# Performance work log

Hardware: AMD Instinct MI355X
Metric: run time of the kernel (lower is better)

Reference implementation:

```python
import jax, jax.numpy as jnp
import numpy as np

D_MODEL = 512
D_INNER = 1024   # expand * d_model
NH = 16          # heads (headdim 64)
HD = 64
NS = 16          # d_state
HID = 1024       # ff hidden = expand * d_model


def _ln(x, w, b, eps=1e-5):
    m = x.mean(-1, keepdims=True)
    v = ((x - m) ** 2).mean(-1, keepdims=True)
    return (x - m) * jax.lax.rsqrt(v + eps) * w + b


def _rms(x, w, eps=1e-5):
    return x * jax.lax.rsqrt((x * x).mean(-1, keepdims=True) + eps) * w


def _tree_scan(dt, xh, Bv, Cv, pidx, A):
    # dt:[B,T,W,H] xh:[B,T,W,H,P] Bv,Cv:[B,T,W,N] pidx:[B,T,W] A:[H]
    B_, T, W, H = dt.shape
    P = xh.shape[-1]
    N = Bv.shape[-1]
    h0 = jnp.zeros((B_, W, H, P, N), dt.dtype)
    xs = (jnp.moveaxis(dt, 1, 0), jnp.moveaxis(xh, 1, 0),
          jnp.moveaxis(Bv, 1, 0), jnp.moveaxis(Cv, 1, 0),
          jnp.moveaxis(pidx, 1, 0))

    def step(h, inp):
        dt_t, xh_t, b_t, c_t, p_t = inp
        # gather parent state from previous level along the width axis
        hp = jnp.take_along_axis(h, p_t[:, :, None, None, None], axis=1)  # [B,W,H,P,N]
        dA = jnp.exp(dt_t * A)                                            # [B,W,H]
        h_new = dA[..., None, None] * hp \
              + dt_t[..., None, None] * xh_t[..., None] * b_t[:, :, None, None, :]
        y_t = jnp.einsum('bwhpn,bwn->bwhp', h_new, c_t)
        return h_new, y_t

    _, ys = jax.lax.scan(step, h0, xs)
    return jnp.moveaxis(ys, 0, 1)  # [B,T,W,H,P]


def setup_inputs() -> dict:
    key = jax.random.key(0)
    ks = jax.random.split(key, 12)
    B, T, W = 8, 64, 16
    d_in_proj = 2 * D_INNER + 2 * NS + NH  # z | x | B | C | dt
    inp = {
        'x': jax.random.normal(ks[0], (B, T, W, D_MODEL), jnp.float32),
        'parent_pos': jax.random.randint(ks[1], (B, T, W), 0, W, dtype=jnp.int32),
        'ln1_w': jnp.ones((D_MODEL,), jnp.float32),
        'ln1_b': jnp.zeros((D_MODEL,), jnp.float32),
        'in_w': jax.random.normal(ks[2], (D_MODEL, d_in_proj), jnp.float32) * 0.02,
        'in_b': jnp.zeros((d_in_proj,), jnp.float32),
        'A_log': jnp.log(jax.random.uniform(ks[3], (NH,), jnp.float32, 1.0, 16.0)),
        'dt_bias': jnp.full((NH,), -4.0, jnp.float32),
        'Dp': jnp.ones((NH,), jnp.float32),
        'norm_w': jnp.ones((D_INNER,), jnp.float32),
        'out_w': jax.random.normal(ks[4], (D_INNER, D_MODEL), jnp.float32) * 0.02,
        'out_b': jnp.zeros((D_MODEL,), jnp.float32),
        'ln2_w': jnp.ones((D_MODEL,), jnp.float32),
        'ln2_b': jnp.zeros((D_MODEL,), jnp.float32),
        'ff1_w': jax.random.normal(ks[5], (D_MODEL, 2 * HID), jnp.float32) * 0.02,
        'ff1_b': jnp.zeros((2 * HID,), jnp.float32),
        'ff2_w': jax.random.normal(ks[6], (HID, D_MODEL), jnp.float32) * 0.02,
        'ff2_b': jnp.zeros((D_MODEL,), jnp.float32),
    }
    return inp


def reference(x, parent_pos, ln1_w, ln1_b, in_w, in_b, A_log, dt_bias, Dp,
              norm_w, out_w, out_b, ln2_w, ln2_b, ff1_w, ff1_b, ff2_w, ff2_b):
    # norm1 + TreeMamba2 + residual
    xn = _ln(x, ln1_w, ln1_b)
    proj = xn @ in_w + in_b
    z, xp, Bv, Cv, dtr = jnp.split(
        proj, [D_INNER, 2 * D_INNER, 2 * D_INNER + NS, 2 * D_INNER + 2 * NS], axis=-1)
    dt = jax.nn.softplus(dtr + dt_bias)            # [B,T,W,NH]
    A = -jnp.exp(A_log)                            # [NH]
    xh = xp.reshape(*xp.shape[:-1], NH, HD)        # [B,T,W,NH,HD]
    y = _tree_scan(dt, xh, Bv, Cv, parent_pos, A)  # [B,T,W,NH,HD]
    y = y + Dp[..., None] * xh                     # skip connection D*x
    y = y.reshape(*y.shape[:-2], D_INNER)
    y = _rms(y * jax.nn.silu(z), norm_w)           # gated RMSNorm
    y = y @ out_w + out_b
    x = y + x
    # norm2 + gated FF + residual
    yn = _ln(x, ln2_w, ln2_b)
    f = yn @ ff1_w + ff1_b
    f1, g = jnp.split(f, 2, axis=-1)
    f = (f1 * jax.nn.silu(g)) @ ff2_w + ff2_b
    return x + f
```

## Files before the change

kernel.cpp:

```cpp
#include <hip/hip_runtime.h>
#include <hip/hip_bf16.h>
#include <cmath>

#define D_MODEL 512
#define D_INNER 1024
#define NHEAD 16
#define HDIM 64
#define NSTATE 16
#define NB 8
#define NT 64
#define NW 16
#define MROWS 8192
#define NPROJ 2096

typedef __attribute__((ext_vector_type(8))) short short8;
typedef __attribute__((ext_vector_type(4))) float f32x4;
typedef __hip_bfloat16 bf16;
typedef unsigned int u32;
typedef unsigned short u16;

__device__ __forceinline__ u32 fbits(float f) { return __float_as_uint(f); }
__device__ __forceinline__ float ubits(u32 u) { return __uint_as_float(u); }
__device__ __forceinline__ u32 pack_bf(float a, float b) {
  return (fbits(b) & 0xffff0000u) | (fbits(a) >> 16);
}

template<int N> __device__ __forceinline__ void vmwait() {
  if constexpr (N == 0)      asm volatile("s_waitcnt vmcnt(0)" ::: "memory");
  else if constexpr (N == 2) asm volatile("s_waitcnt vmcnt(2)" ::: "memory");
  else if constexpr (N == 3) asm volatile("s_waitcnt vmcnt(3)" ::: "memory");
  else if constexpr (N == 4) asm volatile("s_waitcnt vmcnt(4)" ::: "memory");
  else if constexpr (N == 6) asm volatile("s_waitcnt vmcnt(6)" ::: "memory");
  else if constexpr (N == 8) asm volatile("s_waitcnt vmcnt(8)" ::: "memory");
  else static_assert(N == 0, "unsupported vmcnt");
}

__device__ __forceinline__ void xcd_tile(int& bx, int& by) {
  int gx = gridDim.x;
  int nwg = gx * gridDim.y;
  int id = blockIdx.y * gx + blockIdx.x;
  int tile = (id & 7) * (nwg >> 3) + (id >> 3);
  bx = tile % gx;
  by = tile / gx;
}

__device__ __forceinline__ float block_sum(float v, float* sbuf) {
#pragma unroll
  for (int o = 32; o > 0; o >>= 1) v += __shfl_down(v, o, 64);
  int lane = threadIdx.x & 63, wid = threadIdx.x >> 6;
  if (lane == 0) sbuf[wid] = v;
  __syncthreads();
  if (threadIdx.x == 0) {
    float t = 0.f;
    for (int i = 0; i < 4; i++) t += sbuf[i];
    sbuf[0] = t;
  }
  __syncthreads();
  return sbuf[0];
}

__global__ __launch_bounds__(256) void ln512_bf16_kernel(
    const float* __restrict__ x, const float* __restrict__ w,
    const float* __restrict__ b, bf16* __restrict__ out) {
  __shared__ float s1[8], s2[8];
  int row = blockIdx.x;
  const float* xr = x + (size_t)row * D_MODEL;
  bf16* outr = out + (size_t)row * D_MODEL;
  int c0 = threadIdx.x, c1 = threadIdx.x + 256;
  float v0 = xr[c0], v1 = xr[c1];
  float s  = block_sum(v0 + v1, s1);
  float ss = block_sum(v0 * v0 + v1 * v1, s2);
  float mean = s * (1.f / 512.f);
  float var  = ss * (1.f / 512.f) - mean * mean;
  float inv  = rsqrtf(var + 1e-5f);
  outr[c0] = __float2bfloat16((v0 - mean) * inv * w[c0] + b[c0]);
  outr[c1] = __float2bfloat16((v1 - mean) * inv * w[c1] + b[c1]);
}

__global__ __launch_bounds__(256) void wconv_all_kernel(
    const float* __restrict__ in_w, bf16* __restrict__ in_wt,
    const float* __restrict__ out_w, bf16* __restrict__ out_wt,
    const float* __restrict__ ff1_w, bf16* __restrict__ ff1_wt,
    const float* __restrict__ ff2_w, bf16* __restrict__ ff2_wt) {
  __shared__ float tile[32][33];
  int id = blockIdx.x;
  const float* w; bf16* wt;
  int K, N, Npad, bx, by;
  if (id < 1088)      { w = in_w;  wt = in_wt;  K = 512;  N = NPROJ; Npad = 2176; bx = id % 68;  by = id / 68; }
  else if (id < 1600) { int j = id - 1088; w = out_w; wt = out_wt; K = 1024; N = 512;  Npad = 512;  bx = j % 16; by = j / 16; }
  else if (id < 2624) { int j = id - 1600; w = ff1_w; wt = ff1_wt; K = 512;  N = 2048; Npad = 2048; bx = j % 64; by = j / 64; }
  else                { int j = id - 2624; w = ff2_w; wt = ff2_wt; K = 1024; N = 512;  Npad = 512;  bx = j % 16; by = j / 16; }
  int n0 = bx * 32, k0 = by * 32;
  int tx = threadIdx.x & 31, ty = threadIdx.x >> 5;
#pragma unroll
  for (int i = 0; i < 4; i++) {
    int k = k0 + ty + i * 8, n = n0 + tx;
    tile[ty + i * 8][tx] = (k < K && n < N) ? w[(size_t)k * N + n] : 0.f;
  }
  __syncthreads();
#pragma unroll
  for (int i = 0; i < 4; i++) {
    int n = n0 + ty + i * 8, k = k0 + tx;
    if (n < Npad && k < K)
      wt[(size_t)n * K + k] = __float2bfloat16(tile[tx][ty + i * 8]);
  }
}

template<int BM, int BN, int WN, int MR, int NR>
__global__ __launch_bounds__(256) void mfma_gemm_kernel(
    const bf16* __restrict__ A, const bf16* __restrict__ Bt,
    const float* __restrict__ bias, int nbias,
    const float* __restrict__ resid,
    float* __restrict__ C, int ldc, int K) {
  constexpr int ROWS = BM + BN;
  constexpr int ISS  = ROWS / 64;
  __shared__ __align__(16) bf16 sAB[3][ROWS][32];

  int wid = threadIdx.x >> 6, lane = threadIdx.x & 63;
  int bx, by;
  xcd_tile(bx, by);
  int row0 = by * BM, col0 = bx * BN;
  int wr = (wid / WN) * (MR * 16);
  int wc = (wid % WN) * (NR * 16);
  int lr = lane >> 2;
  int lc = (lane & 3) * 8;

  f32x4 acc[MR][NR];
#pragma unroll
  for (int m = 0; m < MR; m++)
#pragma unroll
    for (int n = 0; n < NR; n++) acc[m][n] = (f32x4){0.f, 0.f, 0.f, 0.f};

  auto stage = [&](int buf, int k0) {
#pragma unroll
    for (int i = 0; i < ISS; i++) {
      int rb = (wid * ISS + i) * 16;
      int r = rb + lr;
      const bf16* src = (r < BM)
          ? A  + (size_t)(row0 + r) * K + k0 + lc
          : Bt + (size_t)(col0 + (r - BM)) * K + k0 + lc;
      __builtin_amdgcn_global_load_lds(
          (const __attribute__((address_space(1))) void*)src,
          (__attribute__((address_space(3))) void*)&sAB[buf][rb][0], 16, 0, 0);
    }
  };

  stage(0, 0);
  stage(1, 32);
  int cur = 0;
  for (int k0 = 0; k0 < K; k0 += 32) {
    if (k0 + 32 < K) vmwait<ISS>(); else vmwait<0>();
    __builtin_amdgcn_s_barrier();
    asm volatile("" ::: "memory");
    if (k0 + 64 < K) stage(cur == 0 ? 2 : cur - 1, k0 + 64);
    short8 a[MR], b[NR];
    int kk = (lane >> 4) * 8;
#pragma unroll
    for (int m = 0; m < MR; m++)
      a[m] = *(const short8*)&sAB[cur][wr + m * 16 + (lane & 15)][kk];
#pragma unroll
    for (int n = 0; n < NR; n++)
      b[n] = *(const short8*)&sAB[cur][BM + wc + n * 16 + (lane & 15)][kk];
#pragma unroll
    for (int m = 0; m < MR; m++)
#pragma unroll
      for (int n = 0; n < NR; n++)
        acc[m][n] = __builtin_amdgcn_mfma_f32_16x16x32_bf16(a[m], b[n], acc[m][n], 0, 0, 0);
    asm volatile("" ::: "memory");
    cur = (cur == 2) ? 0 : cur + 1;
  }

  int crow = row0 + wr + (lane >> 4) * 4;
  int ccol = col0 + wc + (lane & 15);
#pragma unroll
  for (int m = 0; m < MR; m++) {
#pragma unroll
    for (int n = 0; n < NR; n++) {
      int colg = ccol + n * 16;
      float bv = bias ? ((colg < nbias) ? bias[colg] : 0.f) : 0.f;
#pragma unroll
      for (int j = 0; j < 4; j++) {
        int rowg = crow + m * 16 + j;
        float v = acc[m][n][j] + bv;
        if (resid) v += resid[(size_t)rowg * ldc + colg];
        C[(size_t)rowg * ldc + colg] = v;
      }
    }
  }
}

__global__ __launch_bounds__(256) void inproj_gemm_kernel(
    const bf16* __restrict__ A, const bf16* __restrict__ Bt,
    const float* __restrict__ bias,
    bf16* __restrict__ zb, bf16* __restrict__ xsc,
    float* __restrict__ aux, int K) {
  constexpr int BM = 128, ROWS = 256, ISS = 4;
  __shared__ __align__(16) bf16 sAB[3][ROWS][32];

  int wid = threadIdx.x >> 6, lane = threadIdx.x & 63;
  int bx, by;
  xcd_tile(bx, by);
  int row0 = by * BM, col0 = bx * 128;
  int wr = (wid >> 1) * 64;
  int wc = (wid & 1) * 64;
  int lr = lane >> 2;
  int lc = (lane & 3) * 8;

  f32x4 acc[4][4];
#pragma unroll
  for (int m = 0; m < 4; m++)
#pragma unroll
    for (int n = 0; n < 4; n++) acc[m][n] = (f32x4){0.f, 0.f, 0.f, 0.f};

  auto stage = [&](int buf, int k0) {
#pragma unroll
    for (int i = 0; i < ISS; i++) {
      int rb = (wid * ISS + i) * 16;
      int r = rb + lr;
      const bf16* src = (r < BM)
          ? A  + (size_t)(row0 + r) * K + k0 + lc
          : Bt + (size_t)(col0 + (r - BM)) * K + k0 + lc;
      __builtin_amdgcn_global_load_lds(
          (const __attribute__((address_space(1))) void*)src,
          (__attribute__((address_space(3))) void*)&sAB[buf][rb][0], 16, 0, 0);
    }
  };

  stage(0, 0);
  stage(1, 32);
  int cur = 0;
  for (int k0 = 0; k0 < K; k0 += 32) {
    if (k0 + 32 < K) vmwait<ISS>(); else vmwait<0>();
    __builtin_amdgcn_s_barrier();
    asm volatile("" ::: "memory");
    if (k0 + 64 < K) stage(cur == 0 ? 2 : cur - 1, k0 + 64);
    short8 a[4], b[4];
    int kk = (lane >> 4) * 8;
#pragma unroll
    for (int m = 0; m < 4; m++)
      a[m] = *(const short8*)&sAB[cur][wr + m * 16 + (lane & 15)][kk];
#pragma unroll
    for (int n = 0; n < 4; n++)
      b[n] = *(const short8*)&sAB[cur][BM + wc + n * 16 + (lane & 15)][kk];
#pragma unroll
    for (int m = 0; m < 4; m++)
#pragma unroll
      for (int n = 0; n < 4; n++)
        acc[m][n] = __builtin_amdgcn_mfma_f32_16x16x32_bf16(a[m], b[n], acc[m][n], 0, 0, 0);
    asm volatile("" ::: "memory");
    cur = (cur == 2) ? 0 : cur + 1;
  }

  int crow = row0 + wr + (lane >> 4) * 4;
  int ccol = col0 + wc + (lane & 15);
#pragma unroll
  for (int m = 0; m < 4; m++) {
#pragma unroll
    for (int n = 0; n < 4; n++) {
      int colg = ccol + n * 16;
      float bv = (colg < NPROJ) ? bias[colg] : 0.f;
#pragma unroll
      for (int j = 0; j < 4; j++) {
        int rowg = crow + m * 16 + j;
        float v = acc[m][n][j] + bv;
        if (colg < 1024) {
          zb[(size_t)rowg * 1024 + colg] = __float2bfloat16(v);
        } else if (colg < 2048) {
          int cx = colg - 1024;
          int h = cx >> 6, p = cx & 63;
          int bb = rowg >> 10, t = (rowg >> 4) & 63, w = rowg & 15;
          size_t idx = ((((size_t)bb * 16 + h) * 4 + (p >> 4)) * 64 + t) * 256
                     + w * 16 + (p & 15);
          xsc[idx] = __float2bfloat16(v);
        } else if (colg < 2112) {
          aux[(size_t)rowg * 64 + (colg - 2048)] = v;
        }
      }
    }
  }
}

__global__ __launch_bounds__(256) void ff1_fused_kernel(
    const bf16* __restrict__ A, const bf16* __restrict__ Bt,
    const float* __restrict__ bias, bf16* __restrict__ out, int K) {
  constexpr int BM = 128, ROWS = 384, ISS = 6;
  __shared__ __align__(16) bf16 sAB[3][ROWS][32];

  int wid = threadIdx.x >> 6, lane = threadIdx.x & 63;
  int bx, by;
  xcd_tile(bx, by);
  int row0 = by * BM, col0 = bx * 128;
  int wr = (wid >> 1) * 64;
  int wc = (wid & 1) * 64;
  int lr = lane >> 2;
  int lc = (lane & 3) * 8;

  f32x4 acc1[4][4], acc2[4][4];
#pragma unroll
  for (int m = 0; m < 4; m++)
#pragma unroll
    for (int n = 0; n < 4; n++) {
      acc1[m][n] = (f32x4){0.f, 0.f, 0.f, 0.f};
      acc2[m][n] = (f32x4){0.f, 0.f, 0.f, 0.f};
    }

  auto stage = [&](int buf, int k0) {
#pragma unroll
    for (int i = 0; i < ISS; i++) {
      int rb = (wid * ISS + i) * 16;
      int r = rb + lr;
      const bf16* src;
      if (r < BM)       src = A  + (size_t)(row0 + r) * K + k0 + lc;
      else if (r < 256) src = Bt + (size_t)(col0 + (r - 128)) * K + k0 + lc;
      else              src = Bt + (size_t)(1024 + col0 + (r - 256)) * K + k0 + lc;
      __builtin_amdgcn_global_load_lds(
          (const __attribute__((address_space(1))) void*)src,
          (__attribute__((address_space(3))) void*)&sAB[buf][rb][0], 16, 0, 0);
    }
  };

  stage(0, 0);
  stage(1, 32);
  int cur = 0;
  for (int k0 = 0; k0 < K; k0 += 32) {
    if (k0 + 32 < K) vmwait<ISS>(); else vmwait<0>();
    __builtin_amdgcn_s_barrier();
    asm volatile("" ::: "memory");
    if (k0 + 64 < K) stage(cur == 0 ? 2 : cur - 1, k0 + 64);
    short8 a[4], b1[4], b2[4];
    int kk = (lane >> 4) * 8;
#pragma unroll
    for (int m = 0; m < 4; m++)
      a[m] = *(const short8*)&sAB[cur][wr + m * 16 + (lane & 15)][kk];
#pragma unroll
    for (int n = 0; n < 4; n++) {
      b1[n] = *(const short8*)&sAB[cur][128 + wc + n * 16 + (lane & 15)][kk];
      b2[n] = *(const short8*)&sAB[cur][256 + wc + n * 16 + (lane & 15)][kk];
    }
#pragma unroll
    for (int m = 0; m < 4; m++)
#pragma unroll
      for (int n = 0; n < 4; n++) {
        acc1[m][n] = __builtin_amdgcn_mfma_f32_16x16x32_bf16(a[m], b1[n], acc1[m][n], 0, 0, 0);
        acc2[m][n] = __builtin_amdgcn_mfma_f32_16x16x32_bf16(a[m], b2[n], acc2[m][n], 0, 0, 0);
      }
    asm volatile("" ::: "memory");
    cur = (cur == 2) ? 0 : cur + 1;
  }

  int crow = row0 + wr + (lane >> 4) * 4;
  int ccol = col0 + wc + (lane & 15);
#pragma unroll
  for (int m = 0; m < 4; m++) {
#pragma unroll
    for (int n = 0; n < 4; n++) {
      int colg = ccol + n * 16;
      float bv1 = bias[colg];
      float bv2 = bias[1024 + colg];
#pragma unroll
      for (int j = 0; j < 4; j++) {
        int rowg = crow + m * 16 + j;
        float f1 = acc1[m][n][j] + bv1;
        float g  = acc2[m][n][j] + bv2;
        float sg = g / (1.f + expf(-g));
        out[(size_t)rowg * 1024 + colg] = __float2bfloat16(f1 * sg);
      }
    }
  }
}

__global__ __launch_bounds__(256) void tree_scan_kernel(
    const bf16* __restrict__ xsc, const float* __restrict__ aux,
    const int* __restrict__ parent,
    const float* __restrict__ A_log, const float* __restrict__ dt_bias,
    const float* __restrict__ Dp, bf16* __restrict__ y) {
  const int tid = threadIdx.x;
  const int ps = blockIdx.x & 3;
  const int h  = (blockIdx.x >> 2) & 15;
  const int b  = blockIdx.x >> 6;
  const int wid = tid >> 6;
  const int lane = tid & 63;
  const int w = lane >> 2;
  const int q = lane & 3;
  const int pl = wid * 4 + q;

  __shared__ __align__(16) u32   BCs[8][16][20];
  __shared__ __align__(16) float dAs[16][8];
  __shared__ __align__(16) float dtss[16][8];
  __shared__ __align__(16) int   pars[16][8];

  const float Ah  = -expf(A_log[h]);
  const float dtb = dt_bias[h];
  const float Dh  = Dp[h];
  const u16* xp = (const u16*)xsc
      + ((((size_t)b * 16 + h) * 4 + ps) * 64) * 256 + w * 16 + pl;
  const int ycol = (h << 6) + (ps << 4) + pl;

  float hst[16];
#pragma unroll
  for (int n = 0; n < 16; n++) hst[n] = 0.f;

  const int sp_t = tid >> 5, sp_w = (tid >> 1) & 15, sp_h = tid & 1;
  const int dt_t = tid >> 4, dt_w = tid & 15;

  u16 xpre[8];
  float4 bc0, bc1, bc2, bc3;
  float dtpre = 0.f;
  int papre = 0;

  auto issue = [&](int c) {
    const int t0 = c * 8;
#pragma unroll
    for (int tt = 0; tt < 8; tt++) xpre[tt] = xp[(size_t)(t0 + tt) * 256];
    size_t row = ((size_t)(b * NT + t0 + sp_t)) * NW + sp_w;
    const float* src = aux + row * 64 + sp_h * 16;
    bc0 = *(const float4*)&src[0];
    bc1 = *(const float4*)&src[4];
    bc2 = *(const float4*)&src[8];
    bc3 = *(const float4*)&src[12];
    if (tid < 128) {
      size_t r2 = ((size_t)(b * NT + t0 + dt_t)) * NW + dt_w;
      dtpre = aux[r2 * 64 + 32 + h];
      papre = parent[r2];
    }
  };

  issue(0);
  for (int c = 0; c < 8; c++) {
    const int t0 = c * 8;
    __syncthreads();
    float xv[8];
#pragma unroll
    for (int tt = 0; tt < 8; tt++) xv[tt] = ubits((u32)xpre[tt] << 16);
    if (tid < 128) {
      float dtr = dtpre + dtb;
      float dtv = (dtr > 20.f) ? dtr : log1pf(expf(dtr));
      dtss[dt_w][dt_t] = dtv;
      dAs[dt_w][dt_t]  = expf(dtv * Ah);
      pars[dt_w][dt_t] = papre;
    }
    {
      uint4 p0 = {pack_bf(bc0.x, bc0.y), pack_bf(bc0.z, bc0.w),
                  pack_bf(bc1.x, bc1.y), pack_bf(bc1.z, bc1.w)};
      uint4 p1 = {pack_bf(bc2.x, bc2.y), pack_bf(bc2.z, bc2.w),
                  pack_bf(bc3.x, bc3.y), pack_bf(bc3.z, bc3.w)};
      *(uint4*)&BCs[sp_t][sp_w][sp_h * 8]     = p0;
      *(uint4*)&BCs[sp_t][sp_w][sp_h * 8 + 4] = p1;
    }
    __syncthreads();
    float dAr[8], dtr8[8];
    int parr[8];
    *(float4*)&dAr[0]  = *(const float4*)&dAs[w][0];
    *(float4*)&dAr[4]  = *(const float4*)&dAs[w][4];
    *(float4*)&dtr8[0] = *(const float4*)&dtss[w][0];
    *(float4*)&dtr8[4] = *(const float4*)&dtss[w][4];
    *(int4*)&parr[0]   = *(const int4*)&pars[w][0];
    *(int4*)&parr[4]   = *(const int4*)&pars[w][4];
    if (c < 7) issue(c + 1);

#pragma unroll
    for (int tt = 0; tt < 8; tt++) {
      float dA  = dAr[tt];
      float dtx = dtr8[tt] * xv[tt];
      int   par = parr[tt];
      int gidx = (((par << 2) | q) << 2);
      u32 pk[8];
#pragma unroll
      for (int i = 0; i < 8; i++)
        pk[i] = (u32)__builtin_amdgcn_ds_bpermute(
            gidx, (int)pack_bf(hst[2 * i], hst[2 * i + 1]));
      uint4 bA = *(const uint4*)&BCs[tt][w][0];
      uint4 bB = *(const uint4*)&BCs[tt][w][4];
      uint4 cA = *(const uint4*)&BCs[tt][w][8];
      uint4 cB = *(const uint4*)&BCs[tt][w][12];
      u32 bwv[8] = {bA.x, bA.y, bA.z, bA.w, bB.x, bB.y, bB.z, bB.w};
      u32 cwv[8] = {cA.x, cA.y, cA.z, cA.w, cB.x, cB.y, cB.z, cB.w};
      float yv = 0.f;
#pragma unroll
      for (int i = 0; i < 8; i++) {
        u32 g = pk[i], bu = bwv[i], cu = cwv[i];
        float hp0 = ubits(g << 16);
        float hp1 = ubits(g & 0xffff0000u);
        float bl  = ubits(bu << 16), bh  = ubits(bu & 0xffff0000u);
        float cl  = ubits(cu << 16), ch  = ubits(cu & 0xffff0000u);
        float h0 = fmaf(dA, hp0, dtx * bl);
        float h1 = fmaf(dA, hp1, dtx * bh);
        hst[2 * i] = h0;
        hst[2 * i + 1] = h1;
        yv = fmaf(h0, cl, fmaf(h1, ch, yv));
      }
      size_t row = ((size_t)(b * NT + t0 + tt)) * NW + w;
      y[row * D_INNER + ycol] = __float2bfloat16(fmaf(Dh, xv[tt], yv));
    }
  }
}

__global__ __launch_bounds__(256) void gate_rms_kernel(
    const bf16* __restrict__ yin, const bf16* __restrict__ zb,
    const float* __restrict__ norm_w, bf16* __restrict__ out) {
  __shared__ float sbuf[8];
  int row = blockIdx.x;
  const bf16* yr = yin + (size_t)row * D_INNER;
  const bf16* zr = zb + (size_t)row * D_INNER;
  int c = threadIdx.x * 4;
  bf16 y4[4], z4[4];
  *(uint2*)y4 = *(const uint2*)&yr[c];
  *(uint2*)z4 = *(const uint2*)&zr[c];
  float gv[4];
  float ss = 0.f;
#pragma unroll
  for (int j = 0; j < 4; j++) {
    float z = __bfloat162float(z4[j]);
    float t = __bfloat162float(y4[j]) * (z / (1.f + expf(-z)));
    gv[j] = t;
    ss += t * t;
  }
  ss = block_sum(ss, sbuf);
  float scale = rsqrtf(ss * (1.f / 1024.f) + 1e-5f);
  bf16 o4[4];
#pragma unroll
  for (int j = 0; j < 4; j++) o4[j] = __float2bfloat16(gv[j] * scale * norm_w[c + j]);
  *(uint2*)&out[(size_t)row * D_INNER + c] = *(uint2*)o4;
}

extern "C" void kernel_launch(void* const* d_in, const int* in_sizes, int n_in,
                              void* d_out, int out_size, void* d_ws, size_t ws_size,
                              hipStream_t stream) {
  const float* x       = (const float*)d_in[0];
  const int*   parent  = (const int*)d_in[1];
  const float* ln1_w   = (const float*)d_in[2];
  const float* ln1_b   = (const float*)d_in[3];
  const float* in_w    = (const float*)d_in[4];
  const float* in_b    = (const float*)d_in[5];
  const float* A_log   = (const float*)d_in[6];
  const float* dt_bias = (const float*)d_in[7];
  const float* Dp      = (const float*)d_in[8];
  const float* norm_w  = (const float*)d_in[9];
  const float* out_w   = (const float*)d_in[10];
  const float* out_b   = (const float*)d_in[11];
  const float* ln2_w   = (const float*)d_in[12];
  const float* ln2_b   = (const float*)d_in[13];
  const float* ff1_w   = (const float*)d_in[14];
  const float* ff1_b   = (const float*)d_in[15];
  const float* ff2_w   = (const float*)d_in[16];
  const float* ff2_b   = (const float*)d_in[17];
  float* outp = (float*)d_out;

  char* wp = (char*)d_ws;
  bf16* xnb    = (bf16*)wp;  wp += (size_t)MROWS * D_MODEL * 2;
  bf16* in_wt  = (bf16*)wp;  wp += (size_t)2176 * D_MODEL * 2;
  bf16* out_wt = (bf16*)wp;  wp += (size_t)D_MODEL * D_INNER * 2;
  bf16* ff1_wt = (bf16*)wp;  wp += (size_t)2048 * D_MODEL * 2;
  bf16* ff2_wt = (bf16*)wp;  wp += (size_t)D_MODEL * D_INNER * 2;
  bf16* zb     = (bf16*)wp;  wp += (size_t)MROWS * D_INNER * 2;
  bf16* xsc    = (bf16*)wp;  wp += (size_t)MROWS * D_INNER * 2;
  float* aux   = (float*)wp; wp += (size_t)MROWS * 64 * 4;
  bf16* yb     = (bf16*)wp;  wp += (size_t)MROWS * D_INNER * 2;
  bf16* ygb    = (bf16*)wp;  wp += (size_t)MROWS * D_INNER * 2;
  float* xmid  = outp;

  dim3 blk(256);
  wconv_all_kernel<<<3136, blk, 0, stream>>>(
      in_w, in_wt, out_w, out_wt, ff1_w, ff1_wt, ff2_w, ff2_wt);
  ln512_bf16_kernel<<<MROWS, blk, 0, stream>>>(x, ln1_w, ln1_b, xnb);
  inproj_gemm_kernel<<<dim3(2176 / 128, MROWS / 128), blk, 0, stream>>>(
      xnb, in_wt, in_b, zb, xsc, aux, D_MODEL);
  tree_scan_kernel<<<NB * NHEAD * 4, blk, 0, stream>>>(xsc, aux, parent,
                                                       A_log, dt_bias, Dp, yb);
  gate_rms_kernel<<<MROWS, blk, 0, stream>>>(yb, zb, norm_w, ygb);
  mfma_gemm_kernel<64, 128, 4, 4, 2><<<dim3(D_MODEL / 128, MROWS / 64), blk, 0, stream>>>(
      ygb, out_wt, out_b, D_MODEL, x, xmid, D_MODEL, D_INNER);
  ln512_bf16_kernel<<<MROWS, blk, 0, stream>>>(xmid, ln2_w, ln2_b, xnb);
  ff1_fused_kernel<<<dim3(8, MROWS / 128), blk, 0, stream>>>(
      xnb, ff1_wt, ff1_b, yb, D_MODEL);
  mfma_gemm_kernel<64, 128, 4, 4, 2><<<dim3(D_MODEL / 128, MROWS / 64), blk, 0, stream>>>(
      yb, ff2_wt, ff2_b, D_MODEL, xmid, outp, D_MODEL, D_INNER);
}
```

Measured before the change: 196.8 us.

## Fuse weight conversion with LN1 and double tree-scan chunk length

```diff
diff --git a/kernel.cpp b/kernel.cpp
--- a/kernel.cpp
+++ b/kernel.cpp
@@ -59,11 +59,10 @@
   return sbuf[0];
 }
 
-__global__ __launch_bounds__(256) void ln512_bf16_kernel(
+__device__ __forceinline__ void ln512_body(
     const float* __restrict__ x, const float* __restrict__ w,
-    const float* __restrict__ b, bf16* __restrict__ out) {
-  __shared__ float s1[8], s2[8];
-  int row = blockIdx.x;
+    const float* __restrict__ b, bf16* __restrict__ out, int row,
+    float* s1, float* s2) {
   const float* xr = x + (size_t)row * D_MODEL;
   bf16* outr = out + (size_t)row * D_MODEL;
   int c0 = threadIdx.x, c1 = threadIdx.x + 256;
@@ -77,13 +76,26 @@
   outr[c1] = __float2bfloat16((v1 - mean) * inv * w[c1] + b[c1]);
 }
 
-__global__ __launch_bounds__(256) void wconv_all_kernel(
+__global__ __launch_bounds__(256) void ln512_bf16_kernel(
+    const float* __restrict__ x, const float* __restrict__ w,
+    const float* __restrict__ b, bf16* __restrict__ out) {
+  __shared__ float s1[8], s2[8];
+  ln512_body(x, w, b, out, blockIdx.x, s1, s2);
+}
+
+__global__ __launch_bounds__(256) void prep_kernel(
     const float* __restrict__ in_w, bf16* __restrict__ in_wt,
     const float* __restrict__ out_w, bf16* __restrict__ out_wt,
     const float* __restrict__ ff1_w, bf16* __restrict__ ff1_wt,
-    const float* __restrict__ ff2_w, bf16* __restrict__ ff2_wt) {
+    const float* __restrict__ ff2_w, bf16* __restrict__ ff2_wt,
+    const float* __restrict__ x, const float* __restrict__ ln1_w,
+    const float* __restrict__ ln1_b, bf16* __restrict__ xnb) {
   __shared__ float tile[32][33];
   int id = blockIdx.x;
+  if (id >= 3136) {
+    ln512_body(x, ln1_w, ln1_b, xnb, id - 3136, &tile[0][0], &tile[1][0]);
+    return;
+  }
   const float* w; bf16* wt;
   int K, N, Npad, bx, by;
   if (id < 1088)      { w = in_w;  wt = in_wt;  K = 512;  N = NPROJ; Npad = 2176; bx = id % 68;  by = id / 68; }
@@ -384,10 +396,10 @@
   const int q = lane & 3;
   const int pl = wid * 4 + q;
 
-  __shared__ __align__(16) u32   BCs[8][16][20];
-  __shared__ __align__(16) float dAs[16][8];
-  __shared__ __align__(16) float dtss[16][8];
-  __shared__ __align__(16) int   pars[16][8];
+  __shared__ __align__(16) u32   BCs[16][16][20];
+  __shared__ __align__(16) float dAs[16][16];
+  __shared__ __align__(16) float dtss[16][16];
+  __shared__ __align__(16) int   pars[16][16];
 
   const float Ah  = -expf(A_log[h]);
   const float dtb = dt_bias[h];
@@ -400,68 +412,74 @@
 #pragma unroll
   for (int n = 0; n < 16; n++) hst[n] = 0.f;
 
-  const int sp_t = tid >> 5, sp_w = (tid >> 1) & 15, sp_h = tid & 1;
   const int dt_t = tid >> 4, dt_w = tid & 15;
 
-  u16 xpre[8];
-  float4 bc0, bc1, bc2, bc3;
+  u16 xpre[16];
+  float4 bcr[2][4];
   float dtpre = 0.f;
   int papre = 0;
 
   auto issue = [&](int c) {
-    const int t0 = c * 8;
-#pragma unroll
-    for (int tt = 0; tt < 8; tt++) xpre[tt] = xp[(size_t)(t0 + tt) * 256];
-    size_t row = ((size_t)(b * NT + t0 + sp_t)) * NW + sp_w;
-    const float* src = aux + row * 64 + sp_h * 16;
-    bc0 = *(const float4*)&src[0];
-    bc1 = *(const float4*)&src[4];
-    bc2 = *(const float4*)&src[8];
-    bc3 = *(const float4*)&src[12];
-    if (tid < 128) {
-      size_t r2 = ((size_t)(b * NT + t0 + dt_t)) * NW + dt_w;
-      dtpre = aux[r2 * 64 + 32 + h];
-      papre = parent[r2];
-    }
+    const int t0 = c * 16;
+#pragma unroll
+    for (int tt = 0; tt < 16; tt++) xpre[tt] = xp[(size_t)(t0 + tt) * 256];
+#pragma unroll
+    for (int r = 0; r < 2; r++) {
+      int idx = tid + (r << 8);
+      int t = idx >> 5, wv = (idx >> 1) & 15, hf = idx & 1;
+      size_t row = ((size_t)(b * NT + t0 + t)) * NW + wv;
+      const float* src = aux + row * 64 + hf * 16;
+      bcr[r][0] = *(const float4*)&src[0];
+      bcr[r][1] = *(const float4*)&src[4];
+      bcr[r][2] = *(const float4*)&src[8];
+      bcr[r][3] = *(const float4*)&src[12];
+    }
+    size_t r2 = ((size_t)(b * NT + t0 + dt_t)) * NW + dt_w;
+    dtpre = aux[r2 * 64 + 32 + h];
+    papre = parent[r2];
   };
 
   issue(0);
-  for (int c = 0; c < 8; c++) {
-    const int t0 = c * 8;
+  for (int c = 0; c < 4; c++) {
+    const int t0 = c * 16;
     __syncthreads();
-    float xv[8];
-#pragma unroll
-    for (int tt = 0; tt < 8; tt++) xv[tt] = ubits((u32)xpre[tt] << 16);
-    if (tid < 128) {
+    float xv[16];
+#pragma unroll
+    for (int tt = 0; tt < 16; tt++) xv[tt] = ubits((u32)xpre[tt] << 16);
+    {
       float dtr = dtpre + dtb;
       float dtv = (dtr > 20.f) ? dtr : log1pf(expf(dtr));
       dtss[dt_w][dt_t] = dtv;
       dAs[dt_w][dt_t]  = expf(dtv * Ah);
       pars[dt_w][dt_t] = papre;
     }
-    {
-      uint4 p0 = {pack_bf(bc0.x, bc0.y), pack_bf(bc0.z, bc0.w),
-                  pack_bf(bc1.x, bc1.y), pack_bf(bc1.z, bc1.w)};
-      uint4 p1 = {pack_bf(bc2.x, bc2.y), pack_bf(bc2.z, bc2.w),
-                  pack_bf(bc3.x, bc3.y), pack_bf(bc3.z, bc3.w)};
-      *(uint4*)&BCs[sp_t][sp_w][sp_h * 8]     = p0;
-      *(uint4*)&BCs[sp_t][sp_w][sp_h * 8 + 4] = p1;
+#pragma unroll
+    for (int r = 0; r < 2; r++) {
+      int idx = tid + (r << 8);
+      int t = idx >> 5, wv = (idx >> 1) & 15, hf = idx & 1;
+      float4 v0 = bcr[r][0], v1 = bcr[r][1], v2 = bcr[r][2], v3 = bcr[r][3];
+      uint4 p0 = {pack_bf(v0.x, v0.y), pack_bf(v0.z, v0.w),
+                  pack_bf(v1.x, v1.y), pack_bf(v1.z, v1.w)};
+      uint4 p1 = {pack_bf(v2.x, v2.y), pack_bf(v2.z, v2.w),
+                  pack_bf(v3.x, v3.y), pack_bf(v3.z, v3.w)};
+      *(uint4*)&BCs[t][wv][hf * 8]     = p0;
+      *(uint4*)&BCs[t][wv][hf * 8 + 4] = p1;
     }
     __syncthreads();
-    float dAr[8], dtr8[8];
-    int parr[8];
-    *(float4*)&dAr[0]  = *(const float4*)&dAs[w][0];
-    *(float4*)&dAr[4]  = *(const float4*)&dAs[w][4];
-    *(float4*)&dtr8[0] = *(const float4*)&dtss[w][0];
-    *(float4*)&dtr8[4] = *(const float4*)&dtss[w][4];
-    *(int4*)&parr[0]   = *(const int4*)&pars[w][0];
-    *(int4*)&parr[4]   = *(const int4*)&pars[w][4];
-    if (c < 7) issue(c + 1);
-
-#pragma unroll
-    for (int tt = 0; tt < 8; tt++) {
+    float dAr[16], dtr16[16];
+    int parr[16];
+#pragma unroll
+    for (int i = 0; i < 4; i++) {
+      *(float4*)&dAr[i * 4]   = *(const float4*)&dAs[w][i * 4];
+      *(float4*)&dtr16[i * 4] = *(const float4*)&dtss[w][i * 4];
+      *(int4*)&parr[i * 4]    = *(const int4*)&pars[w][i * 4];
+    }
+    if (c < 3) issue(c + 1);
+
+#pragma unroll
+    for (int tt = 0; tt < 16; tt++) {
       float dA  = dAr[tt];
-      float dtx = dtr8[tt] * xv[tt];
+      float dtx = dtr16[tt] * xv[tt];
       int   par = parr[tt];
       int gidx = (((par << 2) | q) << 2);
       u32 pk[8];
@@ -560,9 +578,9 @@
   float* xmid  = outp;
 
   dim3 blk(256);
-  wconv_all_kernel<<<3136, blk, 0, stream>>>(
-      in_w, in_wt, out_w, out_wt, ff1_w, ff1_wt, ff2_w, ff2_wt);
-  ln512_bf16_kernel<<<MROWS, blk, 0, stream>>>(x, ln1_w, ln1_b, xnb);
+  prep_kernel<<<3136 + MROWS, blk, 0, stream>>>(
+      in_w, in_wt, out_w, out_wt, ff1_w, ff1_wt, ff2_w, ff2_wt,
+      x, ln1_w, ln1_b, xnb);
   inproj_gemm_kernel<<<dim3(2176 / 128, MROWS / 128), blk, 0, stream>>>(
       xnb, in_wt, in_b, zb, xsc, aux, D_MODEL);
   tree_scan_kernel<<<NB * NHEAD * 4, blk, 0, stream>>>(xsc, aux, parent,
```

Result: no change. 193.8 us (median of 2 runs) (-1.5%).
